# Kernel optimization log

Hardware: AMD Instinct MI355X
Metric: run time of the kernel (lower is better)

## Reference

```python
import jax, jax.numpy as jnp
import numpy as np

N_NODES = 100000
N_EDGES = 1600000
N_RELS = 19
DIMS = [1, 128, 128, 64]  # in_degree feature -> dims


def setup_inputs() -> dict:
    key = jax.random.key(0)
    ks = jax.random.split(key, 12)
    src = jax.random.randint(ks[0], (N_EDGES,), 0, N_NODES, dtype=jnp.int64)
    dst = jax.random.randint(ks[1], (N_EDGES,), 0, N_NODES, dtype=jnp.int64)
    etypes = jax.random.randint(ks[2], (N_EDGES,), 0, N_RELS, dtype=jnp.int64)
    inp = {"src": src, "dst": dst, "etypes": etypes}
    for i, (din, dout) in enumerate(zip(DIMS[:-1], DIMS[1:])):
        s = 1.0 / np.sqrt(max(din, 1))
        inp[f"W{i}"] = jax.random.normal(ks[3 + 3 * i], (N_RELS, din, dout), jnp.float32) * s
        inp[f"Wloop{i}"] = jax.random.normal(ks[4 + 3 * i], (din, dout), jnp.float32) * s
        inp[f"b{i}"] = jnp.zeros((dout,), jnp.float32)
    inp["num_nodes"] = N_NODES
    return inp


def _rel_graph_conv(h, src, dst, etypes, W, Wloop, b, num_nodes, activation):
    # per-relation transform of every node: [N, R, dout]
    transformed = jnp.einsum('nd,rdo->nro', h, W)
    # gather message per edge by (src node, edge relation): [E, dout]
    msg = transformed[src, etypes]
    # scatter-sum to destination nodes
    agg = jax.ops.segment_sum(msg, dst, num_segments=num_nodes)
    out = agg + h @ Wloop + b
    if activation is not None:
        out = activation(out)
    return out


def reference(src, dst, etypes, W0, Wloop0, b0, W1, Wloop1, b1, W2, Wloop2, b2, num_nodes):
    # h = g.in_degrees().view(-1, 1).float()
    deg = jax.ops.segment_sum(jnp.ones_like(dst, dtype=jnp.float32), dst,
                              num_segments=num_nodes)
    h = deg[:, None]
    h = _rel_graph_conv(h, src, dst, etypes, W0, Wloop0, b0, num_nodes, jax.nn.relu)
    h = _rel_graph_conv(h, src, dst, etypes, W1, Wloop1, b1, num_nodes, jax.nn.relu)
    h = _rel_graph_conv(h, src, dst, etypes, W2, Wloop2, b2, num_nodes, None)
    return h
```

## Files before the change

kernel.cpp:

```cpp
#include <hip/hip_runtime.h>
#include <hip/hip_bf16.h>
#include <stdint.h>

#define N_NODES 100000
#define N_EDGES 1600000
#define N_RELS  19
#define NQ      4
#define QN      25000
#define QTILES  196
#define NBQ     98
#define NSB     (NQ * NBQ)
#define N_BUCK  (NQ * N_RELS)
#define NBIN    391
#define NGR     8
#define NBK8    (N_BUCK * NGR)
#define NBIN8   (NBIN * NGR)
#define NHC     (N_BUCK + NBIN)
#define NHC2    (2 * NHC)
#define MSGQ    460000
#define NCKQ    3700
#define NCK_TOT 14000
#define EPB     2048
#define S1B     782

typedef __attribute__((ext_vector_type(8))) short bf16x8;
typedef __attribute__((ext_vector_type(4))) float f32x4;
typedef __attribute__((ext_vector_type(4))) int   int4v;

__device__ __forceinline__ unsigned short f2bf(float x) {
  union { float f; unsigned u; } v; v.f = x;
  unsigned r = v.u + 0x7FFF + ((v.u >> 16) & 1);
  return (unsigned short)(r >> 16);
}
__device__ __forceinline__ float bf2f(unsigned short b) {
  union { unsigned u; float f; } v; v.u = ((unsigned)b) << 16; return v.f;
}

__global__ void k_prep_w(const float* W1, const float* W2,
                         const float* Wl1, const float* Wl2,
                         unsigned short* Wt1, unsigned short* Wt2,
                         unsigned short* Wtl1, unsigned short* Wtl2) {
  int i = blockIdx.x * 256 + threadIdx.x;
  const int s1 = N_RELS * 128 * 128;
  const int s2 = N_RELS * 64 * 128;
  const int s3 = 128 * 128;
  const int s4 = 64 * 128;
  if (i < s1) {
    int r = i / (128 * 128); int rem = i % (128 * 128);
    int n = rem / 128, k = rem % 128;
    Wt1[i] = f2bf(W1[((size_t)r * 128 + k) * 128 + n]);
  } else if (i < s1 + s2) {
    int j = i - s1;
    int r = j / (64 * 128); int rem = j % (64 * 128);
    int n = rem / 128, k = rem % 128;
    Wt2[j] = f2bf(W2[((size_t)r * 128 + k) * 64 + n]);
  } else if (i < s1 + s2 + s3) {
    int j = i - s1 - s2; int n = j / 128, k = j % 128;
    Wtl1[j] = f2bf(Wl1[k * 128 + n]);
  } else if (i < s1 + s2 + s3 + s4) {
    int j = i - s1 - s2 - s3; int n = j / 128, k = j % 128;
    Wtl2[j] = f2bf(Wl2[k * 64 + n]);
  }
}

__global__ void k_hist(const int* __restrict__ dst, const int* __restrict__ et,
                       int* __restrict__ bcount8, int* __restrict__ bincount8,
                       int* __restrict__ histAll) {
  __shared__ int hK[N_BUCK], hB[NBIN];
  __shared__ int sb[256];
  int t = threadIdx.x, g = blockIdx.x & (NGR - 1);
  for (int i = t; i < N_BUCK; i += 256) hK[i] = 0;
  for (int i = t; i < NBIN; i += 256) hB[i] = 0;
  __syncthreads();
  int e0 = blockIdx.x * EPB;
  for (int r = 0; r < EPB / 256; r++) {
    int e = e0 + r * 256 + t;
    if (e < N_EDGES) {
      int d = dst[e];
      atomicAdd(&hK[(d / QN) * N_RELS + et[e]], 1);
      atomicAdd(&hB[d >> 8], 1);
    }
  }
  __syncthreads();
  int* hout = histAll + (size_t)blockIdx.x * NHC2;
  for (int i = t; i < N_BUCK; i += 256) {
    hout[i] = hK[i];
    if (hK[i]) atomicAdd(&bcount8[i * NGR + g], hK[i]);
  }
  for (int i = t; i < NBIN; i += 256) {
    hout[N_BUCK + i] = hB[i];
    if (hB[i]) atomicAdd(&bincount8[i * NGR + g], hB[i]);
  }
  {
    int v0 = (2 * t < N_BUCK) ? hK[2 * t] : 0;
    int v1 = (2 * t + 1 < N_BUCK) ? hK[2 * t + 1] : 0;
    sb[t] = v0 + v1;
    __syncthreads();
    for (int s = 1; s < 256; s <<= 1) {
      int x = (t >= s) ? sb[t - s] : 0;
      __syncthreads();
      sb[t] += x;
      __syncthreads();
    }
    int base = sb[t] - v0 - v1;
    if (2 * t < N_BUCK) hout[NHC + 2 * t] = base;
    if (2 * t + 1 < N_BUCK) hout[NHC + 2 * t + 1] = base + v0;
    __syncthreads();
  }
  {
    int v0 = (2 * t < NBIN) ? hB[2 * t] : 0;
    int v1 = (2 * t + 1 < NBIN) ? hB[2 * t + 1] : 0;
    sb[t] = v0 + v1;
    __syncthreads();
    for (int s = 1; s < 256; s <<= 1) {
      int x = (t >= s) ? sb[t - s] : 0;
      __syncthreads();
      sb[t] += x;
      __syncthreads();
    }
    int base = sb[t] - v0 - v1;
    if (2 * t < NBIN) hout[NHC + N_BUCK + 2 * t] = base;
    if (2 * t + 1 < NBIN) hout[NHC + N_BUCK + 2 * t + 1] = base + v0;
  }
}

__global__ void k_scan0(const int* __restrict__ bcount8, const int* __restrict__ bincount8,
                        int* boff, int* bcur8, int* cbase, int* qcs, int* selfb,
                        int* binoff8, int* bincur8) {
  __shared__ int shK[NBK8];
  __shared__ int sb76[N_BUCK];
  __shared__ int sbs[N_BUCK];
  __shared__ int sh[512];
  int t = threadIdx.x;
  for (int i = t; i < NBK8; i += 512) shK[i] = bcount8[i];
  __syncthreads();
  if (t < N_BUCK) {
    int s = 0;
    for (int gg = 0; gg < NGR; gg++) s += shK[t * NGR + gg];
    sb76[t] = s;
  }
  __syncthreads();
  if (t == 0) {
    int a = 0, cb = 0;
    for (int q = 0; q < NQ; q++) {
      qcs[q] = cb;
      for (int r = 0; r < N_RELS; r++) {
        int b = q * N_RELS + r;
        boff[b] = a; sbs[b] = a; cbase[b] = cb;
        a += sb76[b]; cb += (sb76[b] + 127) >> 7;
      }
      selfb[q] = cb; cb += QTILES;
    }
    qcs[NQ] = cb;
    boff[N_BUCK] = a;
  }
  __syncthreads();
  for (int i = t; i < NBK8; i += 512) {
    int b = i >> 3, gg = i & (NGR - 1);
    int base = sbs[b];
    for (int k = 0; k < gg; k++) base += shK[b * NGR + k];
    bcur8[i] = base;
  }
  int vals[7];
  int i0 = t * 7;
  int loc = 0;
  for (int k = 0; k < 7; k++) {
    int i = i0 + k;
    int v = (i < NBIN8) ? bincount8[i] : 0;
    vals[k] = v; loc += v;
  }
  sh[t] = loc;
  __syncthreads();
  for (int s = 1; s < 512; s <<= 1) {
    int x = (t >= s) ? sh[t - s] : 0;
    __syncthreads();
    sh[t] += x;
    __syncthreads();
  }
  int run = sh[t] - loc;
  for (int k = 0; k < 7; k++) {
    int i = i0 + k;
    if (i < NBIN8) { binoff8[i] = run; bincur8[i] = run; run += vals[k]; }
  }
  if (t == 511) binoff8[NBIN8] = sh[511];
}

__launch_bounds__(256)
__global__ void k_scat1a(const int* __restrict__ src, const int* __restrict__ dst,
                         const int* __restrict__ et,
                         const int* __restrict__ histAll,
                         int* __restrict__ bcur8,
                         int* __restrict__ srcS, int* __restrict__ posE) {
  __shared__ int sortK[EPB];
  __shared__ int lK[N_BUCK], gKr[N_BUCK];
  int t = threadIdx.x, blk = blockIdx.x, g = blk & (NGR - 1);
  const int* hin = histAll + (size_t)blk * NHC2;
  for (int i = t; i < N_BUCK; i += 256) {
    int h = hin[i], l = hin[NHC + i];
    lK[i] = l;
    gKr[i] = h ? (atomicAdd(&bcur8[i * NGR + g], h) - l) : 0;
  }
  __syncthreads();
  int e0 = blk * EPB;
  int nval = min(EPB, N_EDGES - e0);
  for (int r = 0; r < EPB / 256; r++) {
    int e = e0 + r * 256 + t;
    if (e < N_EDGES) {
      int d = dst[e], rl = et[e], sv = src[e];
      int bk = (d / QN) * N_RELS + rl;
      int lrk = atomicAdd(&lK[bk], 1);
      sortK[lrk] = sv | (bk << 17);
      posE[e] = gKr[bk] + lrk;
    }
  }
  __syncthreads();
  for (int r = 0; r < EPB / 256; r++) {
    int s = r * 256 + t;
    if (s < nval) {
      int v = sortK[s];
      srcS[gKr[v >> 17] + s] = v & 0x1FFFF;
    }
  }
}

__launch_bounds__(256)
__global__ void k_scat1b(const int* __restrict__ src, const int* __restrict__ dst,
                         const int* __restrict__ et,
                         const int* __restrict__ posE,
                         const int* __restrict__ histAll,
                         int* __restrict__ bincur8,
                         int* __restrict__ stgA, int* __restrict__ stgB) {
  __shared__ int sortA[EPB], sortBv[EPB];
  __shared__ int lB[NBIN], gBr[NBIN];
  int t = threadIdx.x, blk = blockIdx.x, g = blk & (NGR - 1);
  const int* hin = histAll + (size_t)blk * NHC2;
  for (int i = t; i < NBIN; i += 256) {
    int h = hin[N_BUCK + i], l = hin[NHC + N_BUCK + i];
    lB[i] = l;
    gBr[i] = h ? (atomicAdd(&bincur8[i * NGR + g], h) - l) : 0;
  }
  __syncthreads();
  int e0 = blk * EPB;
  int nval = min(EPB, N_EDGES - e0);
  for (int r = 0; r < EPB / 256; r++) {
    int e = e0 + r * 256 + t;
    if (e < N_EDGES) {
      int d = dst[e], rl = et[e], sv = src[e];
      int gpos = posE[e];
      int bn = d >> 8;
      int lrb = atomicAdd(&lB[bn], 1);
      sortA[lrb] = gpos | (rl << 21) | ((bn & 63) << 26);
      sortBv[lrb] = sv | ((d & 255) << 17) | ((bn >> 6) << 25);
    }
  }
  __syncthreads();
  for (int r = 0; r < EPB / 256; r++) {
    int s = r * 256 + t;
    if (s < nval) {
      int a = sortA[s], b = sortBv[s];
      int bn = ((a >> 26) & 63) | (((b >> 25) & 7) << 6);
      int adr = gBr[bn] + s;
      stgA[adr] = a & 0x03FFFFFF;
      stgB[adr] = b & 0x01FFFFFF;
    }
  }
}

__global__ void k_cnt(const int* __restrict__ stgB, const int* __restrict__ binoff8,
                      int* __restrict__ ncount) {
  __shared__ int c[256];
  int b = blockIdx.x, t = threadIdx.x;
  c[t] = 0;
  __syncthreads();
  int lo = binoff8[b * NGR], hi = binoff8[b * NGR + NGR];
  for (int s = lo + t; s < hi; s += 256)
    atomicAdd(&c[(stgB[s] >> 17) & 255], 1);
  __syncthreads();
  int n = b * 256 + t;
  if (n < N_NODES) ncount[n] = c[t];
}

__global__ void k_scanA(const int* __restrict__ ncount, int* __restrict__ bsum) {
  __shared__ int sh[256];
  int b = blockIdx.x, t = threadIdx.x;
  int q = b / NBQ, bb = b % NBQ;
  int i = bb * 256 + t;
  int val = (i < QN) ? (ncount[q * QN + i] + 1) : 0;
  sh[t] = val;
  __syncthreads();
  for (int s = 128; s > 0; s >>= 1) {
    if (t < s) sh[t] += sh[t + s];
    __syncthreads();
  }
  if (t == 0) bsum[b] = sh[0];
}

__global__ void k_scanB(const int* bsum, int* bbase, int* nodeoff) {
  __shared__ int sh[NSB];
  int t = threadIdx.x;
  if (t < NSB) sh[t] = bsum[t];
  __syncthreads();
  if (t < NQ) {
    int a = 0;
    for (int i = 0; i < NBQ; i++) {
      int v = sh[t * NBQ + i]; sh[t * NBQ + i] = a; a += v;
    }
    nodeoff[(t + 1) * QN + t] = a;
  }
  __syncthreads();
  if (t < NSB) bbase[t] = sh[t];
}

__global__ void k_scanC(const int* __restrict__ ncount,
                        const int* __restrict__ bbase,
                        const int* __restrict__ boff,
                        int* __restrict__ nodeoff, int* __restrict__ ginv) {
  __shared__ int sh[256];
  int b = blockIdx.x, t = threadIdx.x;
  int q = b / NBQ, bb = b % NBQ;
  int i = bb * 256 + t;
  int val = (i < QN) ? (ncount[q * QN + i] + 1) : 0;
  sh[t] = val;
  __syncthreads();
  for (int s = 1; s < 256; s <<= 1) {
    int x = (t >= s) ? sh[t - s] : 0;
    __syncthreads();
    sh[t] += x;
    __syncthreads();
  }
  int excl = sh[t] - val + bbase[b];
  if (i < QN) {
    int n = q * QN + i;
    nodeoff[n + q] = excl;
    int qedges = boff[(q + 1) * N_RELS] - boff[q * N_RELS];
    ginv[(size_t)q * MSGQ + excl] = qedges + i;
  }
}

__global__ void k_scat2(const int* __restrict__ stgA, const int* __restrict__ stgB,
                        const int* __restrict__ binoff8,
                        const int* __restrict__ nodeoff,
                        const int* __restrict__ boff,
                        int* __restrict__ ginv) {
  __shared__ int cur[256];
  __shared__ int qe0s[NQ + 1];
  int b = blockIdx.x, t = threadIdx.x;
  if (t <= NQ) qe0s[t] = boff[t * N_RELS];
  int n = b * 256 + t;
  if (n < N_NODES) {
    int q = n / QN;
    cur[t] = nodeoff[n + q] + 1;
  }
  __syncthreads();
  int lo = binoff8[b * NGR], hi = binoff8[b * NGR + NGR];
  for (int s = lo + t; s < hi; s += 256) {
    int a = stgA[s], bb = stgB[s];
    int dlow = (bb >> 17) & 255;
    int slot = atomicAdd(&cur[dlow], 1);
    int pos = a & 0x1FFFFF;
    int d = b * 256 + dlow;
    int q = d / QN;
    ginv[(size_t)q * MSGQ + slot] = pos - qe0s[q];
  }
}

__global__ void k_rsum(const int* __restrict__ stgA, const int* __restrict__ stgB,
                       const int* __restrict__ binoff8,
                       const int* __restrict__ ncount,
                       const float* __restrict__ W0,
                       const float* __restrict__ Wl0,
                       const float* __restrict__ b0,
                       unsigned short* __restrict__ h1) {
  __shared__ int R[256][N_RELS];
  __shared__ float W0s[N_RELS * 128];
  __shared__ float wl[128], bb[128];
  int b = blockIdx.x, t = threadIdx.x;
  for (int i = t; i < N_RELS * 128; i += 256) W0s[i] = W0[i];
  if (t < 128) { wl[t] = Wl0[t]; bb[t] = b0[t]; }
#pragma unroll
  for (int r = 0; r < N_RELS; r++) R[t][r] = 0;
  __syncthreads();
  int lo = binoff8[b * NGR], hi = binoff8[b * NGR + NGR];
  for (int s = lo + t; s < hi; s += 256) {
    int a = stgA[s], bv = stgB[s];
    int rel = (a >> 21) & 31;
    int sv = bv & 0x1FFFF;
    int dlow = (bv >> 17) & 255;
    atomicAdd(&R[dlow][rel], ncount[sv]);
  }
  __syncthreads();
  int n = b * 256 + t;
  if (n >= N_NODES) return;
  float rr[N_RELS];
#pragma unroll
  for (int r = 0; r < N_RELS; r++) rr[r] = (float)R[t][r];
  float dn = (float)ncount[n];
  unsigned short* hp = &h1[(size_t)n * 128];
  for (int c0 = 0; c0 < 128; c0 += 8) {
    float acc[8];
#pragma unroll
    for (int j = 0; j < 8; j++) acc[j] = dn * wl[c0 + j] + bb[c0 + j];
    for (int r = 0; r < N_RELS; r++) {
#pragma unroll
      for (int j = 0; j < 8; j++)
        acc[j] += rr[r] * W0s[r * 128 + c0 + j];
    }
    unsigned vs[4];
#pragma unroll
    for (int j = 0; j < 4; j++) {
      float x0 = fmaxf(acc[2 * j], 0.f), x1 = fmaxf(acc[2 * j + 1], 0.f);
      vs[j] = (unsigned)f2bf(x0) | ((unsigned)f2bf(x1) << 16);
    }
    int4v o = {(int)vs[0], (int)vs[1], (int)vs[2], (int)vs[3]};
    *(int4v*)&hp[c0] = o;
  }
}

__global__ void k_fill(const int* boff, const int* cbase,
                       const int* selfb, int* cA, int* cB) {
  int b = blockIdx.x;
  if (b < N_BUCK) {
    int cnt = boff[b + 1] - boff[b], e0 = boff[b], w0 = cbase[b];
    int rel = b % N_RELS;
    int nch = (cnt + 127) >> 7;
    for (int i = threadIdx.x; i < nch; i += blockDim.x) {
      cA[w0 + i] = (e0 + i * 128) | (rel << 21);
      cB[w0 + i] = min(128, cnt - i * 128);
    }
  } else {
    int q = b - N_BUCK;
    int w0 = selfb[q];
    for (int i = threadIdx.x; i < QTILES; i += blockDim.x) {
      cA[w0 + i] = (i * 128) | (19 << 21);
      cB[w0 + i] = min(128, QN - i * 128);
    }
  }
}

template <int NOUT>
__launch_bounds__(256, NOUT == 64 ? 6 : 4)
__global__ void k_gemm_msg(const unsigned short* __restrict__ hprev,
                           const unsigned short* __restrict__ Wt,
                           const unsigned short* __restrict__ Wtl,
                           const int* __restrict__ qcs, int q,
                           const int* __restrict__ cA,
                           const int* __restrict__ cB,
                           const int* __restrict__ srcS,
                           const int* __restrict__ boff,
                           unsigned short* __restrict__ msg) {
  const int LDK = 136;
  __shared__ __align__(16) unsigned short Bs[NOUT * LDK];

  int cs = qcs[q], ce = qcs[q + 1];
  int w = blockIdx.x;
  if (w >= ce - cs) return;
  w += cs;
  int pa = cA[w];
  int e0 = pa & 0x1FFFFF, rel = pa >> 21;
  int cnt = cB[w];
  bool self = (rel == 19);
  const unsigned short* wsrc = self ? Wtl : (Wt + (size_t)rel * NOUT * 128);
  int qe0 = boff[q * N_RELS];
  int qedges = boff[(q + 1) * N_RELS] - qe0;
  int ppos0 = self ? (qedges + e0) : (e0 - qe0);
  int tid = threadIdx.x;
  const int lane = tid & 63, wid = tid >> 6;

  int rowg[2]; bool valv[2];
#pragma unroll
  for (int fi = 0; fi < 2; fi++) {
    int m = wid * 32 + fi * 16 + (lane & 15);
    bool v = m < cnt;
    valv[fi] = v;
    int row = 0;
    if (v) row = self ? (q * QN + e0 + m) : srcS[e0 + m];
    rowg[fi] = row;
  }
  bf16x8 a[2][4];
#pragma unroll
  for (int fi = 0; fi < 2; fi++) {
    const unsigned short* rp = hprev + (size_t)rowg[fi] * 128 + (lane >> 4) * 8;
#pragma unroll
    for (int kk = 0; kk < 4; kk++)
      a[fi][kk] = *(const bf16x8*)&rp[kk * 32];
  }
#pragma unroll
  for (int fi = 0; fi < 2; fi++)
    if (!valv[fi]) {
#pragma unroll
      for (int kk = 0; kk < 4; kk++)
        a[fi][kk] = (bf16x8){0, 0, 0, 0, 0, 0, 0, 0};
    }

  for (int task = tid; task < NOUT * 16; task += 256) {
    int n = task >> 4, c = task & 15;
    *(int4v*)&Bs[n * LDK + c * 8] = *(const int4v*)&wsrc[n * 128 + c * 8];
  }
  __syncthreads();

  const int FJ = NOUT / 16;
  f32x4 acc[2][FJ];
#pragma unroll
  for (int i = 0; i < 2; i++)
#pragma unroll
    for (int j = 0; j < FJ; j++) acc[i][j] = (f32x4){0.f, 0.f, 0.f, 0.f};

#pragma unroll
  for (int kk = 0; kk < 4; kk++) {
    int kof = kk * 32 + (lane >> 4) * 8;
    bf16x8 b[FJ];
#pragma unroll
    for (int fj = 0; fj < FJ; fj++)
      b[fj] = *(const bf16x8*)&Bs[(fj * 16 + (lane & 15)) * LDK + kof];
#pragma unroll
    for (int fi = 0; fi < 2; fi++)
#pragma unroll
      for (int fj = 0; fj < FJ; fj++)
        acc[fi][fj] = __builtin_amdgcn_mfma_f32_16x16x32_bf16(a[fi][kk], b[fj], acc[fi][fj], 0, 0, 0);
  }

  __syncthreads();
  unsigned short* Cs = Bs;
#pragma unroll
  for (int fi = 0; fi < 2; fi++)
#pragma unroll
    for (int fj = 0; fj < FJ; fj++)
#pragma unroll
      for (int j = 0; j < 4; j++) {
        int mrow = wid * 32 + fi * 16 + (lane >> 4) * 4 + j;
        int col = fj * 16 + (lane & 15);
        Cs[mrow * NOUT + col] = f2bf(acc[fi][fj][j]);
      }
  __syncthreads();
  const int CW = NOUT / 8;
  for (int task = tid; task < cnt * CW; task += 256) {
    int row = task / CW, c = task % CW;
    *(int4v*)&msg[(size_t)(ppos0 + row) * NOUT + c * 8] =
        *(const int4v*)&Cs[row * NOUT + c * 8];
  }
}

template <int NOUT>
__global__ void k_reduce(const unsigned short* __restrict__ msg,
                         const int* __restrict__ ginv,
                         const int* __restrict__ nodeoff, int q,
                         const float* __restrict__ bias, int do_relu,
                         unsigned short* __restrict__ outh,
                         float* __restrict__ outf) {
  int t = threadIdx.x;
  int rn = blockIdx.x * 8 + (t >> 5);
  if (rn >= QN) return;
  int n = q * QN + rn;
  int l = t & 31;
  int lo = nodeoff[n + q], hi = nodeoff[n + q + 1];
  const int* gv = ginv + (size_t)q * MSGQ;
  if (NOUT == 128) {
    float a0 = 0.f, a1 = 0.f, a2 = 0.f, a3 = 0.f;
    for (int i = lo; i < hi; i++) {
      int ppos = gv[i];
      uint2 v = *(const uint2*)&msg[(size_t)ppos * 128 + l * 4];
      a0 += bf2f((unsigned short)(v.x & 0xffff));
      a1 += bf2f((unsigned short)(v.x >> 16));
      a2 += bf2f((unsigned short)(v.y & 0xffff));
      a3 += bf2f((unsigned short)(v.y >> 16));
    }
    a0 += bias[l * 4];     a1 += bias[l * 4 + 1];
    a2 += bias[l * 4 + 2]; a3 += bias[l * 4 + 3];
    if (do_relu) {
      a0 = fmaxf(a0, 0.f); a1 = fmaxf(a1, 0.f);
      a2 = fmaxf(a2, 0.f); a3 = fmaxf(a3, 0.f);
    }
    uint2 o;
    o.x = (unsigned)f2bf(a0) | ((unsigned)f2bf(a1) << 16);
    o.y = (unsigned)f2bf(a2) | ((unsigned)f2bf(a3) << 16);
    *(uint2*)&outh[(size_t)n * 128 + l * 4] = o;
  } else {
    float a0 = 0.f, a1 = 0.f;
    for (int i = lo; i < hi; i++) {
      int ppos = gv[i];
      unsigned v = *(const unsigned*)&msg[(size_t)ppos * 64 + l * 2];
      a0 += bf2f((unsigned short)(v & 0xffff));
      a1 += bf2f((unsigned short)(v >> 16));
    }
    a0 += bias[l * 2];
    a1 += bias[l * 2 + 1];
    if (do_relu) { a0 = fmaxf(a0, 0.f); a1 = fmaxf(a1, 0.f); }
    outf[(size_t)n * 64 + l * 2]     = a0;
    outf[(size_t)n * 64 + l * 2 + 1] = a1;
  }
}

extern "C" void kernel_launch(void* const* d_in, const int* in_sizes, int n_in,
                              void* d_out, int out_size, void* d_ws, size_t ws_size,
                              hipStream_t stream) {
  const int* src = (const int*)d_in[0];
  const int* dst = (const int*)d_in[1];
  const int* et  = (const int*)d_in[2];
  const float* W0  = (const float*)d_in[3];
  const float* Wl0 = (const float*)d_in[4];
  const float* b0  = (const float*)d_in[5];
  const float* W1  = (const float*)d_in[6];
  const float* Wl1 = (const float*)d_in[7];
  const float* b1  = (const float*)d_in[8];
  const float* W2  = (const float*)d_in[9];
  const float* Wl2 = (const float*)d_in[10];
  const float* b2  = (const float*)d_in[11];

  char* ws = (char*)d_ws;
  size_t off = 0;
  auto alloc = [&](size_t bytes) {
    void* p = ws + off;
    off = (off + bytes + 255) & ~(size_t)255;
    return p;
  };
  unsigned short* msg = (unsigned short*)alloc((size_t)MSGQ * 128 * 2);
  unsigned short* h1 = (unsigned short*)alloc((size_t)N_NODES * 128 * 2);
  unsigned short* h2 = (unsigned short*)alloc((size_t)N_NODES * 128 * 2);
  int* srcS = (int*)alloc((size_t)N_EDGES * 4);
  int* stgA = (int*)alloc((size_t)N_EDGES * 4);
  int* stgB = (int*)alloc((size_t)N_EDGES * 4);
  int* posE = (int*)alloc((size_t)N_EDGES * 4);
  int* ginv = (int*)alloc((size_t)NQ * MSGQ * 4);
  int* ncount  = (int*)alloc((size_t)N_NODES * 4);
  int* nodeoff = (int*)alloc((size_t)(N_NODES + NQ + 4) * 4);
  int* histAll = (int*)alloc((size_t)S1B * NHC2 * 4);
  unsigned short* Wt1  = (unsigned short*)alloc((size_t)N_RELS * 128 * 128 * 2);
  unsigned short* Wt2  = (unsigned short*)alloc((size_t)N_RELS * 64 * 128 * 2);
  unsigned short* Wtl1 = (unsigned short*)alloc((size_t)128 * 128 * 2);
  unsigned short* Wtl2 = (unsigned short*)alloc((size_t)64 * 128 * 2);
  int* acc0 = (int*)alloc((size_t)(NBK8 + NBIN8) * 4);
  int* bcount8   = acc0;
  int* bincount8 = acc0 + NBK8;
  int* ints = (int*)alloc(4096);
  int* boff   = ints;
  int* cbase  = ints + 80;
  int* qcs    = ints + 160;
  int* selfb  = ints + 168;
  int* bcur8  = (int*)alloc((size_t)NBK8 * 4);
  int* binoff8 = (int*)alloc((size_t)(NBIN8 + 1) * 4);
  int* bincur8 = (int*)alloc((size_t)NBIN8 * 4);
  int* bsum  = (int*)alloc((size_t)NSB * 4);
  int* bbase = (int*)alloc((size_t)NSB * 4);
  int* cA = (int*)alloc((size_t)NCK_TOT * 4);
  int* cB = (int*)alloc((size_t)NCK_TOT * 4);

  hipMemsetAsync(acc0, 0, (size_t)(NBK8 + NBIN8) * 4, stream);

  k_prep_w<<<1920, 256, 0, stream>>>(W1, W2, Wl1, Wl2, Wt1, Wt2, Wtl1, Wtl2);
  k_hist<<<S1B, 256, 0, stream>>>(dst, et, bcount8, bincount8, histAll);
  k_scan0<<<1, 512, 0, stream>>>(bcount8, bincount8, boff, bcur8, cbase, qcs,
                                 selfb, binoff8, bincur8);
  k_scat1a<<<S1B, 256, 0, stream>>>(src, dst, et, histAll, bcur8, srcS, posE);
  k_scat1b<<<S1B, 256, 0, stream>>>(src, dst, et, posE, histAll, bincur8,
                                    stgA, stgB);
  k_cnt<<<NBIN, 256, 0, stream>>>(stgB, binoff8, ncount);
  k_scanA<<<NSB, 256, 0, stream>>>(ncount, bsum);
  k_scanB<<<1, 512, 0, stream>>>(bsum, bbase, nodeoff);
  k_scanC<<<NSB, 256, 0, stream>>>(ncount, bbase, boff, nodeoff, ginv);
  k_scat2<<<NBIN, 256, 0, stream>>>(stgA, stgB, binoff8, nodeoff, boff, ginv);
  k_fill<<<N_BUCK + NQ, 256, 0, stream>>>(boff, cbase, selfb, cA, cB);
  k_rsum<<<NBIN, 256, 0, stream>>>(stgA, stgB, binoff8, ncount,
                                   W0, Wl0, b0, h1);

  for (int q = 0; q < NQ; q++) {
    k_gemm_msg<128><<<NCKQ, 256, 0, stream>>>(h1, Wt1, Wtl1, qcs, q, cA, cB,
                                              srcS, boff, msg);
    k_reduce<128><<<QN / 8, 256, 0, stream>>>(msg, ginv, nodeoff, q, b1, 1,
                                              h2, nullptr);
  }
  for (int q = 0; q < NQ; q++) {
    k_gemm_msg<64><<<NCKQ, 256, 0, stream>>>(h2, Wt2, Wtl2, qcs, q, cA, cB,
                                             srcS, boff, msg);
    k_reduce<64><<<QN / 8, 256, 0, stream>>>(msg, ginv, nodeoff, q, b2, 0,
                                             nullptr, (float*)d_out);
  }
}
```

Before: 711.3 us.

## Fuse relation-sum accumulation into scatter kernel and split h1 compute into separate kernel

Moves the per-node per-relation degree-sum accumulation into k_scat2, so the edge staging arrays are read once instead of twice, and writes the sums to a global Rg buffer. A new k_h1 kernel then computes layer-1 features with two threads per node over 782 blocks, stages the bf16 output in shared memory and writes it coalesced. This targets the low parallelism and strided 256-byte-per-thread stores of the old k_rsum. In exchange it adds a 7.6 MB round trip through global memory for Rg and one more launch.

New measurement: 713.9 us. Within noise of the previous version (+0.4%).

```diff
diff --git a/kernel.cpp b/kernel.cpp
--- a/kernel.cpp
+++ b/kernel.cpp
@@ -341,8 +341,10 @@
                         const int* __restrict__ binoff8,
                         const int* __restrict__ nodeoff,
                         const int* __restrict__ boff,
-                        int* __restrict__ ginv) {
+                        const int* __restrict__ ncount,
+                        int* __restrict__ ginv, int* __restrict__ Rg) {
   __shared__ int cur[256];
+  __shared__ int R[256][N_RELS];
   __shared__ int qe0s[NQ + 1];
   int b = blockIdx.x, t = threadIdx.x;
   if (t <= NQ) qe0s[t] = boff[t * N_RELS];
@@ -351,69 +353,74 @@
     int q = n / QN;
     cur[t] = nodeoff[n + q] + 1;
   }
+#pragma unroll
+  for (int r = 0; r < N_RELS; r++) R[t][r] = 0;
   __syncthreads();
   int lo = binoff8[b * NGR], hi = binoff8[b * NGR + NGR];
   for (int s = lo + t; s < hi; s += 256) {
     int a = stgA[s], bb = stgB[s];
     int dlow = (bb >> 17) & 255;
     int slot = atomicAdd(&cur[dlow], 1);
-    int pos = a & 0x1FFFFF;
+    int pos = a & 0x1FFFFF, rel = (a >> 21) & 31;
+    int sv = bb & 0x1FFFF;
     int d = b * 256 + dlow;
     int q = d / QN;
     ginv[(size_t)q * MSGQ + slot] = pos - qe0s[q];
-  }
-}
-
-__global__ void k_rsum(const int* __restrict__ stgA, const int* __restrict__ stgB,
-                       const int* __restrict__ binoff8,
-                       const int* __restrict__ ncount,
-                       const float* __restrict__ W0,
-                       const float* __restrict__ Wl0,
-                       const float* __restrict__ b0,
-                       unsigned short* __restrict__ h1) {
-  __shared__ int R[256][N_RELS];
+    atomicAdd(&R[dlow][rel], ncount[sv]);
+  }
+  __syncthreads();
+  if (n < N_NODES) {
+#pragma unroll
+    for (int r = 0; r < N_RELS; r++)
+      Rg[(size_t)r * N_NODES + n] = R[t][r];
+  }
+}
+
+__launch_bounds__(256, 3)
+__global__ void k_h1(const int* __restrict__ Rg, const int* __restrict__ ncount,
+                     const float* __restrict__ W0, const float* __restrict__ Wl0,
+                     const float* __restrict__ b0,
+                     unsigned short* __restrict__ h1) {
   __shared__ float W0s[N_RELS * 128];
   __shared__ float wl[128], bb[128];
-  int b = blockIdx.x, t = threadIdx.x;
+  __shared__ __align__(16) unsigned short Hs[128 * 128];
+  int t = threadIdx.x, blk = blockIdx.x;
   for (int i = t; i < N_RELS * 128; i += 256) W0s[i] = W0[i];
   if (t < 128) { wl[t] = Wl0[t]; bb[t] = b0[t]; }
-#pragma unroll
-  for (int r = 0; r < N_RELS; r++) R[t][r] = 0;
-  __syncthreads();
-  int lo = binoff8[b * NGR], hi = binoff8[b * NGR + NGR];
-  for (int s = lo + t; s < hi; s += 256) {
-    int a = stgA[s], bv = stgB[s];
-    int rel = (a >> 21) & 31;
-    int sv = bv & 0x1FFFF;
-    int dlow = (bv >> 17) & 255;
-    atomicAdd(&R[dlow][rel], ncount[sv]);
-  }
-  __syncthreads();
-  int n = b * 256 + t;
-  if (n >= N_NODES) return;
-  float rr[N_RELS];
-#pragma unroll
-  for (int r = 0; r < N_RELS; r++) rr[r] = (float)R[t][r];
-  float dn = (float)ncount[n];
-  unsigned short* hp = &h1[(size_t)n * 128];
-  for (int c0 = 0; c0 < 128; c0 += 8) {
-    float acc[8];
-#pragma unroll
-    for (int j = 0; j < 8; j++) acc[j] = dn * wl[c0 + j] + bb[c0 + j];
-    for (int r = 0; r < N_RELS; r++) {
-#pragma unroll
-      for (int j = 0; j < 8; j++)
-        acc[j] += rr[r] * W0s[r * 128 + c0 + j];
-    }
-    unsigned vs[4];
-#pragma unroll
-    for (int j = 0; j < 4; j++) {
-      float x0 = fmaxf(acc[2 * j], 0.f), x1 = fmaxf(acc[2 * j + 1], 0.f);
-      vs[j] = (unsigned)f2bf(x0) | ((unsigned)f2bf(x1) << 16);
-    }
-    int4v o = {(int)vs[0], (int)vs[1], (int)vs[2], (int)vs[3]};
-    *(int4v*)&hp[c0] = o;
-  }
+  __syncthreads();
+  int n0 = blk * 128;
+  int cnt = min(128, N_NODES - n0);
+  int ln = t >> 1;
+  int half = (t & 1) * 64;
+  if (ln < cnt) {
+    int n = n0 + ln;
+    float rr[N_RELS];
+#pragma unroll
+    for (int r = 0; r < N_RELS; r++) rr[r] = (float)Rg[(size_t)r * N_NODES + n];
+    float dn = (float)ncount[n];
+    for (int c0 = half; c0 < half + 64; c0 += 8) {
+      float acc[8];
+#pragma unroll
+      for (int j = 0; j < 8; j++) acc[j] = dn * wl[c0 + j] + bb[c0 + j];
+      for (int r = 0; r < N_RELS; r++) {
+#pragma unroll
+        for (int j = 0; j < 8; j++)
+          acc[j] += rr[r] * W0s[r * 128 + c0 + j];
+      }
+      unsigned vs[4];
+#pragma unroll
+      for (int j = 0; j < 4; j++) {
+        float x0 = fmaxf(acc[2 * j], 0.f), x1 = fmaxf(acc[2 * j + 1], 0.f);
+        vs[j] = (unsigned)f2bf(x0) | ((unsigned)f2bf(x1) << 16);
+      }
+      int4v o = {(int)vs[0], (int)vs[1], (int)vs[2], (int)vs[3]};
+      *(int4v*)&Hs[ln * 128 + c0] = o;
+    }
+  }
+  __syncthreads();
+  int tot = cnt * 16;
+  for (int task = t; task < tot; task += 256)
+    *(int4v*)&h1[(size_t)n0 * 128 + task * 8] = *(const int4v*)&Hs[task * 8];
 }
 
 __global__ void k_fill(const int* boff, const int* cbase,
@@ -621,6 +628,7 @@
   int* stgB = (int*)alloc((size_t)N_EDGES * 4);
   int* posE = (int*)alloc((size_t)N_EDGES * 4);
   int* ginv = (int*)alloc((size_t)NQ * MSGQ * 4);
+  int* Rg   = (int*)alloc((size_t)N_RELS * N_NODES * 4);
   int* ncount  = (int*)alloc((size_t)N_NODES * 4);
   int* nodeoff = (int*)alloc((size_t)(N_NODES + NQ + 4) * 4);
   int* histAll = (int*)alloc((size_t)S1B * NHC2 * 4);
@@ -657,10 +665,10 @@
   k_scanA<<<NSB, 256, 0, stream>>>(ncount, bsum);
   k_scanB<<<1, 512, 0, stream>>>(bsum, bbase, nodeoff);
   k_scanC<<<NSB, 256, 0, stream>>>(ncount, bbase, boff, nodeoff, ginv);
-  k_scat2<<<NBIN, 256, 0, stream>>>(stgA, stgB, binoff8, nodeoff, boff, ginv);
+  k_scat2<<<NBIN, 256, 0, stream>>>(stgA, stgB, binoff8, nodeoff, boff,
+                                    ncount, ginv, Rg);
   k_fill<<<N_BUCK + NQ, 256, 0, stream>>>(boff, cbase, selfb, cA, cB);
-  k_rsum<<<NBIN, 256, 0, stream>>>(stgA, stgB, binoff8, ncount,
-                                   W0, Wl0, b0, h1);
+  k_h1<<<(N_NODES + 127) / 128, 256, 0, stream>>>(Rg, ncount, W0, Wl0, b0, h1);
 
   for (int q = 0; q < NQ; q++) {
     k_gemm_msg<128><<<NCKQ, 256, 0, stream>>>(h1, Wt1, Wtl1, qcs, q, cA, cB,
```
